# Kernel optimization log

Hardware: AMD Instinct MI355X
Metric: run time of the kernel (lower is better)

Reference implementation:

```python
import jax, jax.numpy as jnp
import numpy as np

LOG8 = float(np.log(8.0))


def setup_inputs() -> dict:
    key = jax.random.key(0)
    ks = jax.random.split(key, 5)
    B, T, D = 4, 4096, 1024
    s = 1.0 / float(np.sqrt(D))  # torch default Linear init scale
    return {
        "x": jax.random.normal(ks[0], (B, T, D), dtype=jnp.float32),
        "h": jnp.zeros((B, D), dtype=jnp.float32),
        "W_r": jax.random.uniform(ks[1], (D, D), jnp.float32, -s, s),
        "b_r": jax.random.uniform(ks[2], (D,), jnp.float32, -4.0, -2.0),
        "W_i": jax.random.uniform(ks[3], (D, D), jnp.float32, -s, s),
        "b_i": jnp.zeros((D,), dtype=jnp.float32),
        "W_x": jax.random.uniform(ks[4], (D, D), jnp.float32, -s, s),
    }


def reference(x, h, W_r, b_r, W_i, b_i, W_x):
    # x: (B, T, D); torch Linear is y = x @ W.T + b with W of shape (out, in)
    r = jax.nn.sigmoid(jnp.einsum('btd,ed->bte', x, W_r) + b_r)   # recurrence gate
    i = jax.nn.sigmoid(jnp.einsum('btd,ed->bte', x, W_i) + b_i)   # input gate
    a = jnp.exp(-jax.nn.softplus(LOG8 * r))                        # data-dependent decay in (0,1)
    gate = jnp.sqrt(jnp.clip(1.0 - a * a, 1e-6))
    u = gate * (i * jnp.einsum('btd,ed->bte', x, W_x))             # per-step input term

    # diagonal linear recurrence h_t = a_t * h_{t-1} + u_t, scanned over time
    def step(h_prev, au):
        a_t, u_t = au  # each (B, D)
        h_new = a_t * h_prev + u_t
        return h_new, h_new

    a_t = jnp.swapaxes(a, 0, 1)  # (T, B, D)
    u_t = jnp.swapaxes(u, 0, 1)
    h_last, out = jax.lax.scan(step, h, (a_t, u_t))
    output = jnp.swapaxes(out, 0, 1)  # (B, T, D)
    return output, h_last
```

## Files before the change

### kernel.cpp

```cpp
#include <hip/hip_runtime.h>
#include <stdint.h>

#define D_DIM 1024
#define T_DIM 4096
#define B_DIM 4
#define M_DIM 16384
#define NX 16777216UL
#define NW 1048576UL
#define LOG8F 2.0794415416798357f
#define CHUNK_L 64
#define NCHUNK 64
#define WARM 16

typedef __attribute__((ext_vector_type(4))) float f32x4;
typedef __attribute__((ext_vector_type(8))) short bf16x8;

__device__ __forceinline__ unsigned short f2bf(float f) {
    unsigned u = __float_as_uint(f);
    u += 0x7fffu + ((u >> 16) & 1u);
    return (unsigned short)(u >> 16);
}
__device__ __forceinline__ unsigned packbf2(float x, float y) {
    unsigned ux = __float_as_uint(x);
    ux = (ux + 0x7fffu + ((ux >> 16) & 1u)) >> 16;
    unsigned uy = __float_as_uint(y);
    uy = (uy + 0x7fffu + ((uy >> 16) & 1u)) & 0xffff0000u;
    return ux | uy;
}
__device__ __forceinline__ float unp_lo(unsigned p) { return __uint_as_float(p << 16); }
__device__ __forceinline__ float unp_hi(unsigned p) { return __uint_as_float(p & 0xffff0000u); }
__device__ __forceinline__ float sigm(float x) { return 1.0f / (1.0f + __expf(-x)); }

__device__ __forceinline__ void gl_lds16(const void* g, void* l) {
    __builtin_amdgcn_global_load_lds(
        (const __attribute__((address_space(1))) void*)g,
        (__attribute__((address_space(3))) void*)l, 16, 0, 0);
}

__global__ __launch_bounds__(256) void cvt_kernel(
    const float* __restrict__ x, const float* __restrict__ Wr,
    const float* __restrict__ Wi, const float* __restrict__ Wx,
    unsigned short* __restrict__ xb, unsigned short* __restrict__ wb)
{
    size_t tid = (size_t)blockIdx.x * 256 + threadIdx.x;
    size_t i = tid * 4;
    const float* src;
    unsigned short* dst;
    size_t off;
    if (i < NX) {
        src = x; dst = xb; off = i;
    } else {
        size_t j = i - NX;
        size_t w = j >> 20;
        off = j & (NW - 1);
        src = (w == 0) ? Wr : (w == 1 ? Wi : Wx);
        dst = wb + w * NW;
    }
    float4 v = *(const float4*)(src + off);
    ushort4 o;
    o.x = f2bf(v.x); o.y = f2bf(v.y); o.z = f2bf(v.z); o.w = f2bf(v.w);
    *(ushort4*)(dst + off) = o;
}

__global__ __launch_bounds__(256, 2) void fused_gemm(
    const unsigned short* __restrict__ xb, const unsigned short* __restrict__ wb,
    const float* __restrict__ b_r, const float* __restrict__ b_i,
    unsigned short* __restrict__ a_out, float* __restrict__ u_out)
{
    __shared__ __align__(16) unsigned short As[128 * 32];
    __shared__ __align__(16) unsigned short Bs[2 * 128 * 32];

    const int tid  = threadIdx.x;
    const int lane = tid & 63;
    const int wave = tid >> 6;
    const int wm = wave & 1;
    const int wn = wave >> 1;
    const int m0 = (blockIdx.x >> 3) * 128;
    const int d0 = (blockIdx.x & 7) * 128;
    const int frow = lane & 15;
    const int kgrp = lane >> 4;

    const int r0 = tid >> 2;
    const int c0 = (tid & 3) << 3;
    const unsigned short* xrow = xb + (size_t)m0 * D_DIM;
    const unsigned short* wrow = wb + (size_t)d0 * D_DIM;

    const int mb = m0 + wm * 64;
    const int db = d0 + wn * 64;

    unsigned gip[4][4][2];

    {
        f32x4 acc[2][4][4];
        #pragma unroll
        for (int w = 0; w < 2; w++)
            #pragma unroll
            for (int i = 0; i < 4; i++)
                #pragma unroll
                for (int j = 0; j < 4; j++) acc[w][i][j] = (f32x4){0.f, 0.f, 0.f, 0.f};

        for (int kk = 0; kk < 32; ++kk) {
            const int k0 = kk << 5;
            gl_lds16(xrow + (size_t)r0 * D_DIM + k0 + c0,        &As[tid * 8]);
            gl_lds16(xrow + (size_t)(r0 + 64) * D_DIM + k0 + c0, &As[(tid + 256) * 8]);
            #pragma unroll
            for (int w = 0; w < 2; w++) {
                gl_lds16(wrow + (size_t)w * NW + (size_t)r0 * D_DIM + k0 + c0,
                         &Bs[w * 4096 + tid * 8]);
                gl_lds16(wrow + (size_t)w * NW + (size_t)(r0 + 64) * D_DIM + k0 + c0,
                         &Bs[w * 4096 + (tid + 256) * 8]);
            }
            __syncthreads();
            bf16x8 af[4], bfr[2][4];
            #pragma unroll
            for (int i = 0; i < 4; i++)
                af[i] = *(const bf16x8*)&As[(wm * 64 + i * 16 + frow) * 32 + kgrp * 8];
            #pragma unroll
            for (int w = 0; w < 2; w++)
                #pragma unroll
                for (int j = 0; j < 4; j++)
                    bfr[w][j] = *(const bf16x8*)
                        &Bs[w * 4096 + (wn * 64 + j * 16 + frow) * 32 + kgrp * 8];
            #pragma unroll
            for (int w = 0; w < 2; w++)
                #pragma unroll
                for (int i = 0; i < 4; i++)
                    #pragma unroll
                    for (int j = 0; j < 4; j++)
                        acc[w][i][j] = __builtin_amdgcn_mfma_f32_16x16x32_bf16(
                            af[i], bfr[w][j], acc[w][i][j], 0, 0, 0);
            __syncthreads();
        }

        #pragma unroll
        for (int j = 0; j < 4; j++) {
            const int d = db + j * 16 + frow;
            const float br = b_r[d];
            const float bi = b_i[d];
            #pragma unroll
            for (int i = 0; i < 4; i++) {
                float ig[4];
                #pragma unroll
                for (int r = 0; r < 4; r++) {
                    const int m = mb + i * 16 + kgrp * 4 + r;
                    float rg = sigm(acc[0][i][j][r] + br);
                    float a = sigm(-LOG8F * rg);
                    a_out[(size_t)m * D_DIM + d] = f2bf(a);
                    float g = sqrtf(fmaxf(1.0f - a * a, 1e-6f));
                    ig[r] = g * sigm(acc[1][i][j][r] + bi);
                }
                gip[i][j][0] = packbf2(ig[0], ig[1]);
                gip[i][j][1] = packbf2(ig[2], ig[3]);
            }
        }
    }

    {
        f32x4 acc[4][4];
        #pragma unroll
        for (int i = 0; i < 4; i++)
            #pragma unroll
            for (int j = 0; j < 4; j++) acc[i][j] = (f32x4){0.f, 0.f, 0.f, 0.f};

        const unsigned short* w2 = wrow + 2 * NW;
        for (int kk = 0; kk < 32; ++kk) {
            const int k0 = kk << 5;
            gl_lds16(xrow + (size_t)r0 * D_DIM + k0 + c0,        &As[tid * 8]);
            gl_lds16(xrow + (size_t)(r0 + 64) * D_DIM + k0 + c0, &As[(tid + 256) * 8]);
            gl_lds16(w2 + (size_t)r0 * D_DIM + k0 + c0,          &Bs[tid * 8]);
            gl_lds16(w2 + (size_t)(r0 + 64) * D_DIM + k0 + c0,   &Bs[(tid + 256) * 8]);
            __syncthreads();
            bf16x8 af[4], bfr[4];
            #pragma unroll
            for (int i = 0; i < 4; i++)
                af[i] = *(const bf16x8*)&As[(wm * 64 + i * 16 + frow) * 32 + kgrp * 8];
            #pragma unroll
            for (int j = 0; j < 4; j++)
                bfr[j] = *(const bf16x8*)&Bs[(wn * 64 + j * 16 + frow) * 32 + kgrp * 8];
            #pragma unroll
            for (int i = 0; i < 4; i++)
                #pragma unroll
                for (int j = 0; j < 4; j++)
                    acc[i][j] = __builtin_amdgcn_mfma_f32_16x16x32_bf16(
                        af[i], bfr[j], acc[i][j], 0, 0, 0);
            __syncthreads();
        }

        #pragma unroll
        for (int j = 0; j < 4; j++) {
            const int d = db + j * 16 + frow;
            #pragma unroll
            for (int i = 0; i < 4; i++) {
                #pragma unroll
                for (int r = 0; r < 4; r++) {
                    const int m = mb + i * 16 + kgrp * 4 + r;
                    float gi = (r & 1) ? unp_hi(gip[i][j][r >> 1])
                                       : unp_lo(gip[i][j][r >> 1]);
                    u_out[(size_t)m * D_DIM + d] = gi * acc[i][j][r];
                }
            }
        }
    }
}

__global__ __launch_bounds__(256) void scan_warm(
    const unsigned short* __restrict__ a, const float* __restrict__ u,
    const float* __restrict__ h0, float* __restrict__ hstart)
{
    int tid = blockIdx.x * 256 + threadIdx.x;
    int d = (tid & 511) << 1;
    int bc = tid >> 9;
    int b = bc >> 6;
    int c = bc & (NCHUNK - 1);
    float hx, hy;
    if (c == 0) {
        float2 h = *(const float2*)(h0 + b * D_DIM + d);
        hx = h.x; hy = h.y;
    } else {
        hx = 0.0f; hy = 0.0f;
        size_t base = ((size_t)b * T_DIM + (size_t)c * CHUNK_L - WARM) * D_DIM + d;
        #pragma unroll 4
        for (int t = 0; t < WARM; t++) {
            size_t idx = base + (size_t)t * D_DIM;
            unsigned ap = *(const unsigned*)(a + idx);
            float2 uv = *(const float2*)(u + idx);
            hx = unp_lo(ap) * hx + uv.x;
            hy = unp_hi(ap) * hy + uv.y;
        }
    }
    *(float2*)(hstart + bc * D_DIM + d) = make_float2(hx, hy);
}

__global__ __launch_bounds__(256) void scan_apply(
    const unsigned short* __restrict__ a, const float* __restrict__ hstart,
    float* __restrict__ out)
{
    int tid = blockIdx.x * 256 + threadIdx.x;
    int d = (tid & 511) << 1;
    int bc = tid >> 9;
    int b = bc >> 6;
    int c = bc & (NCHUNK - 1);
    size_t base = ((size_t)b * T_DIM + (size_t)c * CHUNK_L) * D_DIM + d;
    float2 h = *(const float2*)(hstart + bc * D_DIM + d);
    float hx = h.x, hy = h.y;
    #pragma unroll 4
    for (int t = 0; t < CHUNK_L; t++) {
        size_t idx = base + (size_t)t * D_DIM;
        unsigned ap = *(const unsigned*)(a + idx);
        float2 uv = *(const float2*)(out + idx);
        hx = unp_lo(ap) * hx + uv.x;
        hy = unp_hi(ap) * hy + uv.y;
        *(float2*)(out + idx) = make_float2(hx, hy);
    }
    if (c == NCHUNK - 1)
        *(float2*)(out + (size_t)M_DIM * D_DIM + b * D_DIM + d) = make_float2(hx, hy);
}

extern "C" void kernel_launch(void* const* d_in, const int* in_sizes, int n_in,
                              void* d_out, int out_size, void* d_ws, size_t ws_size,
                              hipStream_t stream)
{
    const float* x  = (const float*)d_in[0];
    const float* h0 = (const float*)d_in[1];
    const float* Wr = (const float*)d_in[2];
    const float* br = (const float*)d_in[3];
    const float* Wi = (const float*)d_in[4];
    const float* bi = (const float*)d_in[5];
    const float* Wx = (const float*)d_in[6];
    float* out = (float*)d_out;

    char* ws = (char*)d_ws;
    unsigned short* xb = (unsigned short*)ws;
    unsigned short* wb = (unsigned short*)(ws + 33554432);
    unsigned short* a_buf = (unsigned short*)(ws + 33554432 + 6291456);
    float* hstart = (float*)(ws + 33554432 + 6291456 + 33554432);

    cvt_kernel<<<19456, 256, 0, stream>>>(x, Wr, Wi, Wx, xb, wb);
    fused_gemm<<<1024, 256, 0, stream>>>(xb, wb, br, bi, a_buf, out);
    scan_warm<<<512, 256, 0, stream>>>(a_buf, out, h0, hstart);
    scan_apply<<<512, 256, 0, stream>>>(a_buf, hstart, out);
}
```

Before: 305.0 us.

## Merge three GEMMs into one pipelined K-loop with 4-stage LDS ring

Replaces the two sequential GEMM passes (W_r/W_i, then W_x) with a single K-loop that loads the x tile once and computes all three products together. This removes the second read of x and the bf16 packing of the intermediate gate. The kernel now uses 512 threads and a 4-buffer LDS ring with three stages prefetched, explicit vmcnt waits and a single barrier per tile. LDS reads use an XOR swizzle to avoid bank conflicts, and MFMA sections raise wave priority. In exchange it needs more LDS (128KB per block) and more accumulator registers, which may limit occupancy.

After: 286.6 us. -6.0%, faster.

```diff
diff --git a/kernel.cpp b/kernel.cpp
--- a/kernel.cpp
+++ b/kernel.cpp
@@ -11,6 +11,7 @@
 #define CHUNK_L 64
 #define NCHUNK 64
 #define WARM 16
+#define NT 32
 
 typedef __attribute__((ext_vector_type(4))) float f32x4;
 typedef __attribute__((ext_vector_type(8))) short bf16x8;
@@ -19,13 +20,6 @@
     unsigned u = __float_as_uint(f);
     u += 0x7fffu + ((u >> 16) & 1u);
     return (unsigned short)(u >> 16);
-}
-__device__ __forceinline__ unsigned packbf2(float x, float y) {
-    unsigned ux = __float_as_uint(x);
-    ux = (ux + 0x7fffu + ((ux >> 16) & 1u)) >> 16;
-    unsigned uy = __float_as_uint(y);
-    uy = (uy + 0x7fffu + ((uy >> 16) & 1u)) & 0xffff0000u;
-    return ux | uy;
 }
 __device__ __forceinline__ float unp_lo(unsigned p) { return __uint_as_float(p << 16); }
 __device__ __forceinline__ float unp_hi(unsigned p) { return __uint_as_float(p & 0xffff0000u); }
@@ -62,142 +56,110 @@
     *(ushort4*)(dst + off) = o;
 }
 
-__global__ __launch_bounds__(256, 2) void fused_gemm(
+__global__ __launch_bounds__(512, 2) void fused_gemm(
     const unsigned short* __restrict__ xb, const unsigned short* __restrict__ wb,
     const float* __restrict__ b_r, const float* __restrict__ b_i,
     unsigned short* __restrict__ a_out, float* __restrict__ u_out)
 {
-    __shared__ __align__(16) unsigned short As[128 * 32];
-    __shared__ __align__(16) unsigned short Bs[2 * 128 * 32];
+    __shared__ __align__(16) unsigned short lds[4][4][4096];
 
     const int tid  = threadIdx.x;
     const int lane = tid & 63;
     const int wave = tid >> 6;
     const int wm = wave & 1;
     const int wn = wave >> 1;
-    const int m0 = (blockIdx.x >> 3) * 128;
-    const int d0 = (blockIdx.x & 7) * 128;
+    const int m0 = ((int)blockIdx.x >> 3) * 128;
+    const int d0 = ((int)blockIdx.x & 7) * 128;
     const int frow = lane & 15;
     const int kgrp = lane >> 4;
 
     const int r0 = tid >> 2;
-    const int c0 = (tid & 3) << 3;
-    const unsigned short* xrow = xb + (size_t)m0 * D_DIM;
-    const unsigned short* wrow = wb + (size_t)d0 * D_DIM;
-
-    const int mb = m0 + wm * 64;
-    const int db = d0 + wn * 64;
-
-    unsigned gip[4][4][2];
-
-    {
-        f32x4 acc[2][4][4];
-        #pragma unroll
-        for (int w = 0; w < 2; w++)
-            #pragma unroll
-            for (int i = 0; i < 4; i++)
-                #pragma unroll
-                for (int j = 0; j < 4; j++) acc[w][i][j] = (f32x4){0.f, 0.f, 0.f, 0.f};
-
-        for (int kk = 0; kk < 32; ++kk) {
-            const int k0 = kk << 5;
-            gl_lds16(xrow + (size_t)r0 * D_DIM + k0 + c0,        &As[tid * 8]);
-            gl_lds16(xrow + (size_t)(r0 + 64) * D_DIM + k0 + c0, &As[(tid + 256) * 8]);
-            #pragma unroll
-            for (int w = 0; w < 2; w++) {
-                gl_lds16(wrow + (size_t)w * NW + (size_t)r0 * D_DIM + k0 + c0,
-                         &Bs[w * 4096 + tid * 8]);
-                gl_lds16(wrow + (size_t)w * NW + (size_t)(r0 + 64) * D_DIM + k0 + c0,
-                         &Bs[w * 4096 + (tid + 256) * 8]);
-            }
-            __syncthreads();
-            bf16x8 af[4], bfr[2][4];
-            #pragma unroll
-            for (int i = 0; i < 4; i++)
-                af[i] = *(const bf16x8*)&As[(wm * 64 + i * 16 + frow) * 32 + kgrp * 8];
-            #pragma unroll
-            for (int w = 0; w < 2; w++)
-                #pragma unroll
-                for (int j = 0; j < 4; j++)
-                    bfr[w][j] = *(const bf16x8*)
-                        &Bs[w * 4096 + (wn * 64 + j * 16 + frow) * 32 + kgrp * 8];
-            #pragma unroll
-            for (int w = 0; w < 2; w++)
-                #pragma unroll
-                for (int i = 0; i < 4; i++)
-                    #pragma unroll
-                    for (int j = 0; j < 4; j++)
-                        acc[w][i][j] = __builtin_amdgcn_mfma_f32_16x16x32_bf16(
-                            af[i], bfr[w][j], acc[w][i][j], 0, 0, 0);
-            __syncthreads();
-        }
-
-        #pragma unroll
-        for (int j = 0; j < 4; j++) {
-            const int d = db + j * 16 + frow;
-            const float br = b_r[d];
-            const float bi = b_i[d];
-            #pragma unroll
-            for (int i = 0; i < 4; i++) {
-                float ig[4];
-                #pragma unroll
-                for (int r = 0; r < 4; r++) {
-                    const int m = mb + i * 16 + kgrp * 4 + r;
-                    float rg = sigm(acc[0][i][j][r] + br);
-                    float a = sigm(-LOG8F * rg);
-                    a_out[(size_t)m * D_DIM + d] = f2bf(a);
-                    float g = sqrtf(fmaxf(1.0f - a * a, 1e-6f));
-                    ig[r] = g * sigm(acc[1][i][j][r] + bi);
-                }
-                gip[i][j][0] = packbf2(ig[0], ig[1]);
-                gip[i][j][1] = packbf2(ig[2], ig[3]);
-            }
-        }
-    }
-
-    {
-        f32x4 acc[4][4];
+    const int cgs = (tid & 3) ^ ((r0 >> 1) & 3);
+    const unsigned short* srcA = xb + (size_t)(m0 + r0) * D_DIM + cgs * 8;
+    const unsigned short* srcB = wb + (size_t)(d0 + r0) * D_DIM + cgs * 8;
+
+    int offA[4], offB[2];
+    #pragma unroll
+    for (int i = 0; i < 4; i++) {
+        const int row = wm * 64 + i * 16 + frow;
+        offA[i] = row * 32 + ((kgrp ^ ((row >> 1) & 3)) << 3);
+    }
+    #pragma unroll
+    for (int j = 0; j < 2; j++) {
+        const int row = wn * 32 + j * 16 + frow;
+        offB[j] = row * 32 + ((kgrp ^ ((row >> 1) & 3)) << 3);
+    }
+
+    f32x4 acc[3][4][2];
+    #pragma unroll
+    for (int w = 0; w < 3; w++)
         #pragma unroll
         for (int i = 0; i < 4; i++)
             #pragma unroll
-            for (int j = 0; j < 4; j++) acc[i][j] = (f32x4){0.f, 0.f, 0.f, 0.f};
-
-        const unsigned short* w2 = wrow + 2 * NW;
-        for (int kk = 0; kk < 32; ++kk) {
-            const int k0 = kk << 5;
-            gl_lds16(xrow + (size_t)r0 * D_DIM + k0 + c0,        &As[tid * 8]);
-            gl_lds16(xrow + (size_t)(r0 + 64) * D_DIM + k0 + c0, &As[(tid + 256) * 8]);
-            gl_lds16(w2 + (size_t)r0 * D_DIM + k0 + c0,          &Bs[tid * 8]);
-            gl_lds16(w2 + (size_t)(r0 + 64) * D_DIM + k0 + c0,   &Bs[(tid + 256) * 8]);
-            __syncthreads();
-            bf16x8 af[4], bfr[4];
+            for (int j = 0; j < 2; j++) acc[w][i][j] = (f32x4){0.f, 0.f, 0.f, 0.f};
+
+    auto stage = [&](int t) {
+        const int buf = t & 3;
+        const int k0 = t << 5;
+        gl_lds16(srcA + k0, &lds[buf][0][tid * 8]);
+        #pragma unroll
+        for (int w = 0; w < 3; w++)
+            gl_lds16(srcB + (size_t)w * NW + k0, &lds[buf][1 + w][tid * 8]);
+    };
+
+    stage(0); stage(1); stage(2);
+
+#define TILE_BODY(T, VM)                                                      \
+    {                                                                         \
+        asm volatile("s_waitcnt vmcnt(" #VM ")" ::: "memory");                \
+        __builtin_amdgcn_s_barrier();                                         \
+        if ((T) + 3 < NT) stage((T) + 3);                                     \
+        const int buf = (T) & 3;                                              \
+        bf16x8 af[4], bfr[3][2];                                              \
+        _Pragma("unroll")                                                     \
+        for (int i = 0; i < 4; i++)                                           \
+            af[i] = *(const bf16x8*)&lds[buf][0][offA[i]];                    \
+        _Pragma("unroll")                                                     \
+        for (int w = 0; w < 3; w++)                                           \
+            _Pragma("unroll")                                                 \
+            for (int j = 0; j < 2; j++)                                       \
+                bfr[w][j] = *(const bf16x8*)&lds[buf][1 + w][offB[j]];        \
+        __builtin_amdgcn_s_setprio(1);                                        \
+        _Pragma("unroll")                                                     \
+        for (int w = 0; w < 3; w++)                                           \
+            _Pragma("unroll")                                                 \
+            for (int i = 0; i < 4; i++)                                       \
+                _Pragma("unroll")                                             \
+                for (int j = 0; j < 2; j++)                                   \
+                    acc[w][i][j] = __builtin_amdgcn_mfma_f32_16x16x32_bf16(   \
+                        af[i], bfr[w][j], acc[w][i][j], 0, 0, 0);             \
+        __builtin_amdgcn_s_setprio(0);                                        \
+    }
+
+    for (int t = 0; t < NT - 3; ++t) TILE_BODY(t, 8);
+    TILE_BODY(NT - 3, 8);
+    TILE_BODY(NT - 2, 4);
+    TILE_BODY(NT - 1, 0);
+#undef TILE_BODY
+
+    const int mb = m0 + wm * 64 + kgrp * 4;
+    const int db = d0 + wn * 32 + frow;
+    #pragma unroll
+    for (int j = 0; j < 2; j++) {
+        const int d = db + j * 16;
+        const float br = b_r[d];
+        const float bi = b_i[d];
+        #pragma unroll
+        for (int i = 0; i < 4; i++) {
+            const int m = mb + i * 16;
             #pragma unroll
-            for (int i = 0; i < 4; i++)
-                af[i] = *(const bf16x8*)&As[(wm * 64 + i * 16 + frow) * 32 + kgrp * 8];
-            #pragma unroll
-            for (int j = 0; j < 4; j++)
-                bfr[j] = *(const bf16x8*)&Bs[(wn * 64 + j * 16 + frow) * 32 + kgrp * 8];
-            #pragma unroll
-            for (int i = 0; i < 4; i++)
-                #pragma unroll
-                for (int j = 0; j < 4; j++)
-                    acc[i][j] = __builtin_amdgcn_mfma_f32_16x16x32_bf16(
-                        af[i], bfr[j], acc[i][j], 0, 0, 0);
-            __syncthreads();
-        }
-
-        #pragma unroll
-        for (int j = 0; j < 4; j++) {
-            const int d = db + j * 16 + frow;
-            #pragma unroll
-            for (int i = 0; i < 4; i++) {
-                #pragma unroll
-                for (int r = 0; r < 4; r++) {
-                    const int m = mb + i * 16 + kgrp * 4 + r;
-                    float gi = (r & 1) ? unp_hi(gip[i][j][r >> 1])
-                                       : unp_lo(gip[i][j][r >> 1]);
-                    u_out[(size_t)m * D_DIM + d] = gi * acc[i][j][r];
-                }
+            for (int r = 0; r < 4; r++) {
+                const size_t idx = (size_t)(m + r) * D_DIM + d;
+                float rg = sigm(acc[0][i][j][r] + br);
+                float a = sigm(-LOG8F * rg);
+                a_out[idx] = f2bf(a);
+                float g = sqrtf(fmaxf(1.0f - a * a, 1e-6f));
+                u_out[idx] = g * sigm(acc[1][i][j][r] + bi) * acc[2][i][j][r];
             }
         }
     }
@@ -276,7 +238,7 @@
     float* hstart = (float*)(ws + 33554432 + 6291456 + 33554432);
 
     cvt_kernel<<<19456, 256, 0, stream>>>(x, Wr, Wi, Wx, xb, wb);
-    fused_gemm<<<1024, 256, 0, stream>>>(xb, wb, br, bi, a_buf, out);
+    fused_gemm<<<1024, 512, 0, stream>>>(xb, wb, br, bi, a_buf, out);
     scan_warm<<<512, 256, 0, stream>>>(a_buf, out, h0, hstart);
     scan_apply<<<512, 256, 0, stream>>>(a_buf, hstart, out);
 }
```
